# Optimization experiments

Measured on AMD Instinct MI355X. Metric: run time of the kernel, lower is better.

The kernel has to match this reference:

```python
import jax, jax.numpy as jnp
import numpy as np

EPS = 1e-08


def setup_inputs() -> dict:
    key = jax.random.key(0)
    k1, k2, k3 = jax.random.split(key, 3)
    B, T, IN, OUT = 32, 500, 2048, 1024
    x = jax.random.normal(k1, (B, T, IN), dtype=jnp.float32)
    # torch init: normal(mean=0, std=w_init_std*sqrt(1/input_shape))
    w = jax.random.normal(k2, (IN, OUT), dtype=jnp.float32) * np.sqrt(1.0 / IN)
    # b ~ N(1.0, 0.01), clamped >= 0
    b = jnp.clip(1.0 + 0.01 * jax.random.normal(k3, (OUT,), dtype=jnp.float32), 0.0, None)
    decay_m = jnp.array([0.6], dtype=jnp.float32)  # N(0.6, .01) clamped to [0,1]
    decay_s = jnp.array([0.9], dtype=jnp.float32)  # N(0.9, .01) clamped to [0,1]
    return {"x": x, "w": w, "b": b, "decay_m": decay_m, "decay_s": decay_s}


def reference(x, w, b, decay_m, decay_s):
    # x: [B, T, IN]; w: [IN, OUT]
    B, T, _ = x.shape
    OUT = w.shape[1]
    h = jnp.einsum('btc,cd->btd', x, w)          # [B, T, OUT]
    norm = jnp.sum(w * w, axis=0)                 # [OUT]
    dm = decay_m[0]
    ds = decay_s[0]
    inv_norm = 1.0 / (norm + EPS)
    zeros = jnp.zeros((B, OUT), dtype=x.dtype)
    # spk is never assigned a spike value in the original forward (spike_fn
    # is never applied), so it remains zero throughout.
    spk = zeros

    def step(carry, inp):
        M, S, E = carry
        E = dm * norm * (E + spk)                 # spk == 0 (faithful to source)
        M = dm * (M + inp)
        S = ds * (S + inp)
        mem = M - S - E
        mthr = mem * inv_norm - b                 # [B, OUT]
        return (M, S, E), mthr

    (_, _, _), spk_rec_t = jax.lax.scan(step, (zeros, zeros, zeros),
                                        jnp.swapaxes(h, 0, 1))  # [T, B, OUT]
    spk_rec = jnp.swapaxes(spk_rec_t, 0, 1)       # [B, T, OUT]
    loss = 0.5 * jnp.mean(spk_rec ** 2)
    return (spk_rec, loss)
```

## Files before the change

### kernel.cpp

```cpp
#include <hip/hip_runtime.h>


typedef __bf16 bf16x8 __attribute__((ext_vector_type(8)));
typedef __bf16 bf16x4 __attribute__((ext_vector_type(4)));
typedef float  f32x4  __attribute__((ext_vector_type(4)));

#define BDIM 32
#define TDIM 500
#define INDIM 2048
#define OUTDIM 1024
#define MROWS 16000
#define NCHUNK 25
#define CHLEN 20
#define OUT_ELEMS 16384000

__device__ __forceinline__ void gld_lds16(const void* g, void* l) {
    __builtin_amdgcn_global_load_lds(
        (const __attribute__((address_space(1))) unsigned int*)g,
        (__attribute__((address_space(3))) unsigned int*)l, 16, 0, 0);
}

__global__ void convert_x(const float* __restrict__ x, __bf16* __restrict__ xb) {
    size_t i = ((size_t)blockIdx.x * 256 + threadIdx.x) * 8;
    float4 a = *(const float4*)(x + i);
    float4 b = *(const float4*)(x + i + 4);
    bf16x8 o;
    o[0] = (__bf16)a.x; o[1] = (__bf16)a.y; o[2] = (__bf16)a.z; o[3] = (__bf16)a.w;
    o[4] = (__bf16)b.x; o[5] = (__bf16)b.y; o[6] = (__bf16)b.z; o[7] = (__bf16)b.w;
    *(bf16x8*)(xb + i) = o;
}

__global__ void transpose_w(const float* __restrict__ w, __bf16* __restrict__ wbt,
                            float* __restrict__ normAcc) {
    __shared__ float tile[32][33];
    __shared__ float red[8][33];
    const int tx = threadIdx.x;
    const int ty = threadIdx.y;
    const int d0 = blockIdx.x * 32;
    const int c0 = blockIdx.y * 32;
    float s = 0.f;
#pragma unroll
    for (int i = 0; i < 4; ++i) {
        int c = c0 + ty + i * 8;
        float v = w[(size_t)c * OUTDIM + d0 + tx];
        tile[ty + i * 8][tx] = v;
        s += v * v;
    }
    red[ty][tx] = s;
    __syncthreads();
#pragma unroll
    for (int i = 0; i < 4; ++i) {
        int d = d0 + ty + i * 8;
        wbt[(size_t)d * INDIM + c0 + tx] = (__bf16)tile[tx][ty + i * 8];
    }
    if (ty == 0) {
        float t = red[0][tx] + red[1][tx] + red[2][tx] + red[3][tx]
                + red[4][tx] + red[5][tx] + red[6][tx] + red[7][tx];
        atomicAdd(&normAcc[d0 + tx], t);
    }
}

__global__ __launch_bounds__(256, 2) void gemm_bf16(
    const __bf16* __restrict__ A,
    const __bf16* __restrict__ Bt,
    __bf16* __restrict__ H)
{
    constexpr int K = INDIM;
    __shared__ __align__(16) __bf16 As[128 * 64];
    __shared__ __align__(16) __bf16 Bs[256 * 64];

    const int tid  = threadIdx.x;
    const int wave = tid >> 6;
    const int lane = tid & 63;
    const int bm = blockIdx.y * 128;
    const int bn = blockIdx.x * 256;
    const int wn = wave * 64;

    const int srow8 = lane >> 3;
    const int sseg  = lane & 7;
    const int quad = lane >> 4;
    const int mrow = lane & 15;

    f32x4 acc[8][4] = {};

    for (int k0 = 0; k0 < K; k0 += 64) {
        __syncthreads();
#pragma unroll
        for (int g = 0; g < 4; ++g) {
            const int rbase = wave * 32 + g * 8;
            const int row   = rbase + srow8;
            const int q     = sseg ^ (row & 7);
            gld_lds16(A + (size_t)(bm + row) * K + k0 + q * 8, &As[rbase * 64]);
        }
#pragma unroll
        for (int g = 0; g < 8; ++g) {
            const int rbase = wave * 64 + g * 8;
            const int row   = rbase + srow8;
            const int q     = sseg ^ (row & 7);
            gld_lds16(Bt + (size_t)(bn + row) * K + k0 + q * 8, &Bs[rbase * 64]);
        }
        __syncthreads();

#pragma unroll
        for (int ks = 0; ks < 2; ++ks) {
            bf16x8 af[8], bfr[4];
#pragma unroll
            for (int i = 0; i < 8; ++i) {
                const int r = i * 16 + mrow;
                af[i] = *(const bf16x8*)&As[r * 64 + (((ks * 4 + quad) ^ (r & 7)) * 8)];
            }
#pragma unroll
            for (int j = 0; j < 4; ++j) {
                const int r = wn + j * 16 + mrow;
                bfr[j] = *(const bf16x8*)&Bs[r * 64 + (((ks * 4 + quad) ^ (r & 7)) * 8)];
            }
#pragma unroll
            for (int i = 0; i < 8; ++i)
#pragma unroll
                for (int j = 0; j < 4; ++j)
                    acc[i][j] = __builtin_amdgcn_mfma_f32_16x16x32_bf16(
                        af[i], bfr[j], acc[i][j], 0, 0, 0);
        }
    }

#pragma unroll
    for (int i = 0; i < 8; ++i)
#pragma unroll
        for (int j = 0; j < 4; ++j)
#pragma unroll
            for (int r = 0; r < 4; ++r) {
                const int R = bm + i * 16 + quad * 4 + r;
                const int C = bn + wn + j * 16 + mrow;
                H[(size_t)R * OUTDIM + C] = (__bf16)acc[i][j][r];
            }
}

__global__ void scan1(const __bf16* __restrict__ H,
                      f32x4* __restrict__ cM, f32x4* __restrict__ cS,
                      const float* __restrict__ dmp, const float* __restrict__ dsp) {
    const float dm = *dmp, ds = *dsp;
    const int c = blockIdx.x, b = blockIdx.y, tid = threadIdx.x;
    f32x4 M = {}, S = {};
    const __bf16* p = H + ((size_t)b * TDIM + c * CHLEN) * OUTDIM + tid * 4;
#pragma unroll 4
    for (int t = 0; t < CHLEN; ++t) {
        bf16x4 hv = *(const bf16x4*)(p + (size_t)t * OUTDIM);
        f32x4 h; h[0] = hv[0]; h[1] = hv[1]; h[2] = hv[2]; h[3] = hv[3];
        M = dm * (M + h);
        S = ds * (S + h);
    }
    const size_t idx = ((size_t)c * BDIM + b) * 256 + tid;
    cM[idx] = M;
    cS[idx] = S;
}

__global__ void scan2(float* __restrict__ cM, float* __restrict__ cS,
                      const float* __restrict__ dmp, const float* __restrict__ dsp) {
    const float dm = *dmp, ds = *dsp;
    float km = 1.f, ks = 1.f;
#pragma unroll
    for (int i = 0; i < CHLEN; ++i) { km *= dm; ks *= ds; }
    const int gid = blockIdx.x * 256 + threadIdx.x;
    const int b = gid >> 10, d = gid & 1023;
    float tM = 0.f, tS = 0.f;
    for (int c = 0; c < NCHUNK; ++c) {
        const size_t idx = (((size_t)c * BDIM + b) << 10) + d;
        float oM = cM[idx], oS = cS[idx];
        cM[idx] = tM; cS[idx] = tS;
        tM = km * tM + oM;
        tS = ks * tS + oS;
    }
}

__global__ void scan3(const __bf16* __restrict__ H,
                      const f32x4* __restrict__ cM, const f32x4* __restrict__ cS,
                      const float* __restrict__ normAcc, const float* __restrict__ bias,
                      const float* __restrict__ dmp, const float* __restrict__ dsp,
                      float* __restrict__ out, float* __restrict__ lossAcc,
                      unsigned* __restrict__ ticket) {
    const float dm = *dmp, ds = *dsp;
    const int c = blockIdx.x, b = blockIdx.y, tid = threadIdx.x;
    const size_t cidx = ((size_t)c * BDIM + b) * 256 + tid;
    f32x4 M = cM[cidx];
    f32x4 S = cS[cidx];
    f32x4 nv = *(const f32x4*)(normAcc + tid * 4);
    f32x4 inv;
    inv[0] = 1.f / (nv[0] + 1e-8f); inv[1] = 1.f / (nv[1] + 1e-8f);
    inv[2] = 1.f / (nv[2] + 1e-8f); inv[3] = 1.f / (nv[3] + 1e-8f);
    f32x4 bv = *(const f32x4*)(bias + tid * 4);

    const size_t rowbase = ((size_t)b * TDIM + c * CHLEN) * OUTDIM + tid * 4;
    const __bf16* p = H + rowbase;
    float* o = out + rowbase;
    float loss = 0.f;
#pragma unroll 4
    for (int t = 0; t < CHLEN; ++t) {
        bf16x4 hv = *(const bf16x4*)(p + (size_t)t * OUTDIM);
        f32x4 h; h[0] = hv[0]; h[1] = hv[1]; h[2] = hv[2]; h[3] = hv[3];
        M = dm * (M + h);
        S = ds * (S + h);
        f32x4 r = (M - S) * inv - bv;
        *(f32x4*)(o + (size_t)t * OUTDIM) = r;
        loss += r[0] * r[0] + r[1] * r[1] + r[2] * r[2] + r[3] * r[3];
    }
    __shared__ float red[256];
    red[tid] = loss;
    __syncthreads();
    for (int s = 128; s > 0; s >>= 1) {
        if (tid < s) red[tid] += red[tid + s];
        __syncthreads();
    }
    if (tid == 0) {
        atomicAdd(lossAcc, red[0]);
        __threadfence();
        unsigned t = atomicAdd(ticket, 1u);
        if (t == NCHUNK * BDIM - 1) {
            float total = atomicAdd(lossAcc, 0.0f);
            out[OUT_ELEMS] = 0.5f * total / (float)OUT_ELEMS;
        }
    }
}

#define OFF_H      ((size_t)0)
#define OFF_WBT    ((size_t)32768000)
#define OFF_NORM   ((size_t)36962304)
#define OFF_LOSS   ((size_t)36966400)
#define OFF_TICKET ((size_t)36966404)
#define OFF_CM     ((size_t)36966656)
#define OFF_CS     ((size_t)40243456)

extern "C" void kernel_launch(void* const* d_in, const int* in_sizes, int n_in,
                              void* d_out, int out_size, void* d_ws, size_t ws_size,
                              hipStream_t stream) {
    const float* x  = (const float*)d_in[0];
    const float* w  = (const float*)d_in[1];
    const float* bb = (const float*)d_in[2];
    const float* dm = (const float*)d_in[3];
    const float* ds = (const float*)d_in[4];

    char* ws = (char*)d_ws;
    __bf16*   H    = (__bf16*)(ws + OFF_H);
    __bf16*   WBT  = (__bf16*)(ws + OFF_WBT);
    float*    NORM = (float*)(ws + OFF_NORM);
    float*    LOSS = (float*)(ws + OFF_LOSS);
    unsigned* TICK = (unsigned*)(ws + OFF_TICKET);
    f32x4*    CM   = (f32x4*)(ws + OFF_CM);
    f32x4*    CS   = (f32x4*)(ws + OFF_CS);
    __bf16*   XB   = (__bf16*)d_out;
    float*    out  = (float*)d_out;

    hipMemsetAsync(ws + OFF_NORM, 0, 4096 + 256, stream);

    convert_x<<<16000, 256, 0, stream>>>(x, XB);
    transpose_w<<<dim3(32, 64), dim3(32, 8), 0, stream>>>(w, WBT, NORM);
    gemm_bf16<<<dim3(4, 125), 256, 0, stream>>>(XB, WBT, H);
    scan1<<<dim3(NCHUNK, BDIM), 256, 0, stream>>>(H, CM, CS, dm, ds);
    scan2<<<128, 256, 0, stream>>>((float*)CM, (float*)CS, dm, ds);
    scan3<<<dim3(NCHUNK, BDIM), 256, 0, stream>>>(H, CM, CS, NORM, bb, dm, ds,
                                                  out, LOSS, TICK);
}
```

Baseline: 336.2 us.

## Restructure bf16 GEMM into 256x256 tiles with 4-stage LDS pipeline

Rewrites the GEMM to use 512-thread blocks computing 256x256 output tiles with a four-deep ring of K=32 LDS buffers. Global-to-LDS loads are issued ahead and gated by explicit vmcnt waits. MFMA phases are raised in priority with setprio and separated by barriers. A 1D grid of 252 blocks is remapped by XCD so neighbouring tiles share an XCD, and the last M tile is clamped and masked. This aims to hide load latency and raise reuse, but adds many barriers and leaves a partially wasted final row tile.

```diff
diff --git a/kernel.cpp b/kernel.cpp
--- a/kernel.cpp
+++ b/kernel.cpp
@@ -60,78 +60,109 @@
     }
 }
 
-__global__ __launch_bounds__(256, 2) void gemm_bf16(
+__global__ __launch_bounds__(512, 2) void gemm_bf16(
     const __bf16* __restrict__ A,
     const __bf16* __restrict__ Bt,
     __bf16* __restrict__ H)
 {
-    constexpr int K = INDIM;
-    __shared__ __align__(16) __bf16 As[128 * 64];
-    __shared__ __align__(16) __bf16 Bs[256 * 64];
+    constexpr int K  = INDIM;
+    constexpr int NT = K / 32;
+    __shared__ __align__(16) __bf16 As[4][256 * 32];
+    __shared__ __align__(16) __bf16 Bs[4][256 * 32];
 
     const int tid  = threadIdx.x;
     const int wave = tid >> 6;
     const int lane = tid & 63;
-    const int bm = blockIdx.y * 128;
-    const int bn = blockIdx.x * 256;
-    const int wn = wave * 64;
-
-    const int srow8 = lane >> 3;
-    const int sseg  = lane & 7;
-    const int quad = lane >> 4;
-    const int mrow = lane & 15;
+    const int wm   = wave >> 2;
+    const int wn   = wave & 3;
+
+    const int orig = blockIdx.x;
+    const int xcd = orig & 7, within = orig >> 3;
+    const int wgid = (xcd < 4) ? (xcd * 32 + within)
+                               : (128 + (xcd - 4) * 31 + within);
+    const int bm = (wgid >> 2) * 256;
+    const int bn = (wgid & 3) * 256;
+
+    const int srow = lane >> 2;
+    const int sseg = lane & 3;
+    const int scol = (sseg ^ ((srow >> 1) & 3)) * 8;
+    const int lds0 = (wave * 16) * 32;
+    const int lds1 = (128 + wave * 16) * 32;
+    int rA0 = bm +       wave * 16 + srow; if (rA0 > MROWS - 1) rA0 = MROWS - 1;
+    int rA1 = bm + 128 + wave * 16 + srow; if (rA1 > MROWS - 1) rA1 = MROWS - 1;
+    const __bf16* gA0 = A  + (size_t)rA0 * K + scol;
+    const __bf16* gA1 = A  + (size_t)rA1 * K + scol;
+    const __bf16* gB0 = Bt + (size_t)(bn +       wave * 16 + srow) * K + scol;
+    const __bf16* gB1 = Bt + (size_t)(bn + 128 + wave * 16 + srow) * K + scol;
+
+    const int mrow = lane & 15, quad = lane >> 4;
+    const int swzq = quad ^ ((mrow >> 1) & 3);
+    const int rdA = (wm * 128 + mrow) * 32 + swzq * 8;
+    const int rdB = (wn * 64  + mrow) * 32 + swzq * 8;
 
     f32x4 acc[8][4] = {};
 
-    for (int k0 = 0; k0 < K; k0 += 64) {
-        __syncthreads();
-#pragma unroll
-        for (int g = 0; g < 4; ++g) {
-            const int rbase = wave * 32 + g * 8;
-            const int row   = rbase + srow8;
-            const int q     = sseg ^ (row & 7);
-            gld_lds16(A + (size_t)(bm + row) * K + k0 + q * 8, &As[rbase * 64]);
-        }
-#pragma unroll
-        for (int g = 0; g < 8; ++g) {
-            const int rbase = wave * 64 + g * 8;
-            const int row   = rbase + srow8;
-            const int q     = sseg ^ (row & 7);
-            gld_lds16(Bt + (size_t)(bn + row) * K + k0 + q * 8, &Bs[rbase * 64]);
-        }
-        __syncthreads();
-
-#pragma unroll
-        for (int ks = 0; ks < 2; ++ks) {
-            bf16x8 af[8], bfr[4];
-#pragma unroll
-            for (int i = 0; i < 8; ++i) {
-                const int r = i * 16 + mrow;
-                af[i] = *(const bf16x8*)&As[r * 64 + (((ks * 4 + quad) ^ (r & 7)) * 8)];
-            }
-#pragma unroll
-            for (int j = 0; j < 4; ++j) {
-                const int r = wn + j * 16 + mrow;
-                bfr[j] = *(const bf16x8*)&Bs[r * 64 + (((ks * 4 + quad) ^ (r & 7)) * 8)];
-            }
-#pragma unroll
-            for (int i = 0; i < 8; ++i)
-#pragma unroll
-                for (int j = 0; j < 4; ++j)
-                    acc[i][j] = __builtin_amdgcn_mfma_f32_16x16x32_bf16(
-                        af[i], bfr[j], acc[i][j], 0, 0, 0);
-        }
-    }
-
+#define STAGE(tt) do { const int _b = (tt) & 3; const size_t _k = (size_t)(tt) * 32; \
+        gld_lds16(gA0 + _k, &As[_b][lds0]);                                          \
+        gld_lds16(gA1 + _k, &As[_b][lds1]);                                          \
+        gld_lds16(gB0 + _k, &Bs[_b][lds0]);                                          \
+        gld_lds16(gB1 + _k, &Bs[_b][lds1]); } while (0)
+
+    STAGE(0); STAGE(1); STAGE(2); STAGE(3);
+    asm volatile("s_waitcnt vmcnt(12)" ::: "memory");
+    asm volatile("s_barrier" ::: "memory");
+
+#pragma unroll 1
+    for (int t = 0; t < NT; ++t) {
+        const __bf16* as = As[t & 3];
+        const __bf16* bs = Bs[t & 3];
+        bf16x8 af[4], bfr[4];
+#pragma unroll
+        for (int i = 0; i < 4; ++i) af[i]  = *(const bf16x8*)&as[rdA + i * 512];
+#pragma unroll
+        for (int j = 0; j < 4; ++j) bfr[j] = *(const bf16x8*)&bs[rdB + j * 512];
+        asm volatile("s_barrier" ::: "memory");
+        __builtin_amdgcn_s_setprio(1);
+#pragma unroll
+        for (int i = 0; i < 4; ++i)
+#pragma unroll
+            for (int j = 0; j < 4; ++j)
+                acc[i][j] = __builtin_amdgcn_mfma_f32_16x16x32_bf16(
+                    af[i], bfr[j], acc[i][j], 0, 0, 0);
+        __builtin_amdgcn_s_setprio(0);
+        asm volatile("s_barrier" ::: "memory");
+#pragma unroll
+        for (int i = 0; i < 4; ++i) af[i] = *(const bf16x8*)&as[rdA + 2048 + i * 512];
+        asm volatile("s_barrier" ::: "memory");
+        __builtin_amdgcn_s_setprio(1);
+#pragma unroll
+        for (int i = 0; i < 4; ++i)
+#pragma unroll
+            for (int j = 0; j < 4; ++j)
+                acc[4 + i][j] = __builtin_amdgcn_mfma_f32_16x16x32_bf16(
+                    af[i], bfr[j], acc[4 + i][j], 0, 0, 0);
+        __builtin_amdgcn_s_setprio(0);
+        asm volatile("s_barrier" ::: "memory");
+        if (t + 4 < NT) STAGE(t + 4);
+        if (t < NT - 4)       asm volatile("s_waitcnt vmcnt(12)" ::: "memory");
+        else if (t == NT - 4) asm volatile("s_waitcnt vmcnt(8)"  ::: "memory");
+        else if (t == NT - 3) asm volatile("s_waitcnt vmcnt(4)"  ::: "memory");
+        else if (t == NT - 2) asm volatile("s_waitcnt vmcnt(0)"  ::: "memory");
+        if (t < NT - 1) asm volatile("s_barrier" ::: "memory");
+    }
+#undef STAGE
+
+    const int Rb = bm + wm * 128 + quad * 4;
+    const int Cb = bn + wn * 64 + mrow;
 #pragma unroll
     for (int i = 0; i < 8; ++i)
 #pragma unroll
         for (int j = 0; j < 4; ++j)
 #pragma unroll
             for (int r = 0; r < 4; ++r) {
-                const int R = bm + i * 16 + quad * 4 + r;
-                const int C = bn + wn + j * 16 + mrow;
-                H[(size_t)R * OUTDIM + C] = (__bf16)acc[i][j][r];
+                const int R = Rb + i * 16 + r;
+                if (R < MROWS)
+                    H[(size_t)R * OUTDIM + Cb + j * 16] = (__bf16)acc[i][j][r];
             }
 }
 
@@ -253,7 +284,7 @@
 
     convert_x<<<16000, 256, 0, stream>>>(x, XB);
     transpose_w<<<dim3(32, 64), dim3(32, 8), 0, stream>>>(w, WBT, NORM);
-    gemm_bf16<<<dim3(4, 125), 256, 0, stream>>>(XB, WBT, H);
+    gemm_bf16<<<252, 512, 0, stream>>>(XB, WBT, H);
     scan1<<<dim3(NCHUNK, BDIM), 256, 0, stream>>>(H, CM, CS, dm, ds);
     scan2<<<128, 256, 0, stream>>>((float*)CM, (float*)CS, dm, ds);
     scan3<<<dim3(NCHUNK, BDIM), 256, 0, stream>>>(H, CM, CS, NORM, bb, dm, ds,
```

Result: slower. 361.4 us (+7.5%).
